# Kernel tuning notes

Measured on AMD Instinct MI355X. Metric: run time of the kernel, lower is better.

## Reference

```python
import jax, jax.numpy as jnp
import numpy as np

EPS = 1e-5

def _layer_norm(x, g, b):
    m = jnp.mean(x, axis=-1, keepdims=True)
    v = jnp.mean((x - m) ** 2, axis=-1, keepdims=True)
    return (x - m) / jnp.sqrt(v + EPS) * g + b

def _dpb(idx, w0, b0, g1, be1, w1, b1, g2, be2, w2, b2, g3, be3, w3, b3):
    # idx: (n, dim, 1) -> (h, n, dim)
    h = idx @ w0 + b0                                   # (n, dim, D)
    h = jax.nn.relu(_layer_norm(h, g1, be1)) @ w1 + b1  # pos1
    h = jax.nn.relu(_layer_norm(h, g2, be2)) @ w2 + b2  # pos2
    h = jax.nn.relu(_layer_norm(h, g3, be3)) @ w3 + b3  # pos3 -> (n, dim, H)
    return jnp.transpose(h, (2, 0, 1))                  # (H, n, dim)

def setup_inputs() -> dict:
    key = jax.random.key(0)
    ks = jax.random.split(key, 6)
    B, H, N, DIM, D = 8, 16, 4096, 64, 64
    s = 0.02
    return {
        "x": jax.random.normal(ks[0], (B, H, N, DIM), jnp.float32),
        "w0": jax.random.normal(ks[1], (1, D), jnp.float32) * s,
        "b0": jnp.zeros((D,), jnp.float32),
        "g1": jnp.ones((D,), jnp.float32),
        "be1": jnp.zeros((D,), jnp.float32),
        "w1": jax.random.normal(ks[2], (D, D), jnp.float32) * s,
        "b1": jnp.zeros((D,), jnp.float32),
        "g2": jnp.ones((D,), jnp.float32),
        "be2": jnp.zeros((D,), jnp.float32),
        "w2": jax.random.normal(ks[3], (D, D), jnp.float32) * s,
        "b2": jnp.zeros((D,), jnp.float32),
        "g3": jnp.ones((D,), jnp.float32),
        "be3": jnp.zeros((D,), jnp.float32),
        "w3": jax.random.normal(ks[4], (D, H), jnp.float32) * s,
        "b3": jnp.zeros((H,), jnp.float32),
    }

def reference(x, w0, b0, g1, be1, w1, b1, g2, be2, w2, b2, g3, be3, w3, b3):
    # DynamicToepliztMultiheadV3 forward (par_type=1, no pad/exp/decay, non-causal)
    n = x.shape[-2]
    dim = x.shape[-1]
    m = n - 1
    dpb_args = (w0, b0, g1, be1, w1, b1, g2, be2, w2, b2, g3, be3, w3, b3)
    scale = 1.0 / (m * dim)
    flat = jnp.arange(1, 1 + m * dim, dtype=x.dtype)
    pos_idx = (flat * scale).reshape(m, dim, 1)
    neg_idx = (-jnp.flip(flat) * scale).reshape(m, dim, 1)  # flip on flat, then reshape (matches torch)
    zero_idx = jnp.zeros((1, dim, 1), x.dtype)
    zero = _dpb(zero_idx, *dpb_args)   # (H, 1, dim)
    pos = _dpb(pos_idx, *dpb_args)     # (H, n-1, dim)
    neg = _dpb(neg_idx, *dpb_args)     # (H, n-1, dim)
    a = jnp.concatenate([zero, pos, zero, neg], axis=1)  # (H, 2n, dim)
    # FFT-based circular (Toeplitz) convolution along seq axis
    y = jnp.fft.rfft(x, 2 * n, axis=-2, norm='ortho')          # (B,H,n+1,dim) complex
    v = jnp.fft.rfft(a, axis=-2)[None]                          # backward norm, as in torch
    out = jnp.fft.irfft(v * y, 2 * n, axis=-2, norm='ortho')[:, :, :n, :]
    return out
```

## Files before the change

### kernel.cpp

```cpp
#include <hip/hip_runtime.h>
#include <math.h>

static const size_t OFF_TW = 0;
static const size_t OFF_V  = 32768;
static const size_t OFF_AT = OFF_V  + (size_t)16 * 64 * 4104 * 8;
static const size_t OFF_ZX = OFF_AT + (size_t)16 * 32 * 8192 * 8;
static const size_t WS_NEED = OFF_ZX + (size_t)128 * 32 * 4096 * 8;

__global__ void __launch_bounds__(256) k_init_tw(float2* __restrict__ tw)
{
    int k = blockIdx.x * 256 + threadIdx.x;
    if (k < 4096) {
        double a = (double)k * (3.14159265358979323846 / 4096.0);
        tw[k] = make_float2((float)cos(a), (float)(-sin(a)));
    }
}

__device__ __forceinline__ void ln_relu_arr(float* b,
                                            const float* __restrict__ g,
                                            const float* __restrict__ be)
{
    float s0 = 0, s1 = 0, s2 = 0, s3 = 0;
    #pragma unroll
    for (int k = 0; k < 64; k += 4) {
        s0 += b[k]; s1 += b[k + 1]; s2 += b[k + 2]; s3 += b[k + 3];
    }
    float m = (s0 + s1 + s2 + s3) * (1.0f / 64.0f);
    float v0 = 0, v1 = 0, v2 = 0, v3 = 0;
    #pragma unroll
    for (int k = 0; k < 64; k += 4) {
        float c0 = b[k] - m, c1 = b[k + 1] - m, c2 = b[k + 2] - m, c3 = b[k + 3] - m;
        v0 = fmaf(c0, c0, v0); v1 = fmaf(c1, c1, v1);
        v2 = fmaf(c2, c2, v2); v3 = fmaf(c3, c3, v3);
    }
    float inv = rsqrtf((v0 + v1 + v2 + v3) * (1.0f / 64.0f) + 1e-5f);
    #pragma unroll
    for (int k = 0; k < 64; ++k)
        b[k] = fmaxf(fmaf((b[k] - m) * inv, g[k], be[k]), 0.0f);
}

__device__ __forceinline__ void matmul64(const float* b, float* o,
                                         const float* __restrict__ w,
                                         const float* __restrict__ bias)
{
    #pragma unroll
    for (int j = 0; j < 64; ++j) o[j] = bias[j];
    #pragma unroll
    for (int k = 0; k < 64; ++k) {
        float bk = b[k];
        const float* wr = w + (k << 6);
        #pragma unroll
        for (int j = 0; j < 64; ++j) o[j] = fmaf(bk, wr[j], o[j]);
    }
}

__global__ void __launch_bounds__(256) k_dpb(
    const float* __restrict__ w0,  const float* __restrict__ b0,
    const float* __restrict__ g1,  const float* __restrict__ be1,
    const float* __restrict__ w1,  const float* __restrict__ b1,
    const float* __restrict__ g2,  const float* __restrict__ be2,
    const float* __restrict__ w2,  const float* __restrict__ b2,
    const float* __restrict__ g3,  const float* __restrict__ be3,
    const float* __restrict__ w3,  const float* __restrict__ b3,
    float* __restrict__ aTf)
{
    int e  = blockIdx.x * 256 + threadIdx.x;
    int r  = e & 8191;
    int dd = e >> 13;
    const float scale = (float)(1.0 / 262080.0);
    float u;
    if (r == 0 || r == 4096) u = 0.0f;
    else if (r < 4096)       u = (float)((r - 1) * 64 + dd + 1) * scale;
    else                     u = -(float)(262080 - ((r - 4097) * 64 + dd)) * scale;

    float b[64], o[64];
    #pragma unroll
    for (int j = 0; j < 64; ++j) b[j] = fmaf(u, w0[j], b0[j]);

    ln_relu_arr(b, g1, be1);
    matmul64(b, o, w1, b1);
    ln_relu_arr(o, g2, be2);
    matmul64(o, b, w2, b2);
    ln_relu_arr(b, g3, be3);

    float f[16];
    #pragma unroll
    for (int j = 0; j < 16; ++j) f[j] = b3[j];
    #pragma unroll
    for (int k = 0; k < 64; ++k) {
        float bk = b[k];
        const float* wr = w3 + (k << 4);
        #pragma unroll
        for (int j = 0; j < 16; ++j) f[j] = fmaf(bk, wr[j], f[j]);
    }
    #pragma unroll
    for (int h = 0; h < 16; ++h) {
        size_t idx = ((size_t)((h << 5) + (dd >> 1)) * 8192 + r) * 2 + (dd & 1);
        aTf[idx] = f[h];
    }
}

__device__ __forceinline__ int sw(int a)
{
    return a ^ ((a >> 4) & 15) ^ ((a >> 8) & 1);
}

__device__ __forceinline__ float2 cmul(float2 a, float2 b)
{
    return make_float2(fmaf(a.x, b.x, -(a.y * b.y)), fmaf(a.x, b.y, a.y * b.x));
}

template<bool INV>
__device__ __forceinline__ float2 twm(float2 a, float wr, float wi)
{
    float i = INV ? -wi : wi;
    return make_float2(fmaf(a.x, wr, -(a.y * i)), fmaf(a.x, i, a.y * wr));
}

template<bool INV>
__device__ __forceinline__ void fft16(float2* z)
{
    const float SQ = 0.70710678118654752440f;
    const float C1 = 0.92387953251128675613f;
    const float S1 = 0.38268343236508977173f;
    #pragma unroll
    for (int b = 0; b < 16; b += 2) {
        float2 u = z[b], t = z[b + 1];
        z[b]     = make_float2(u.x + t.x, u.y + t.y);
        z[b + 1] = make_float2(u.x - t.x, u.y - t.y);
    }
    const float w4r[2] = {1.0f, 0.0f};
    const float w4i[2] = {0.0f, -1.0f};
    #pragma unroll
    for (int b = 0; b < 16; b += 4) {
        #pragma unroll
        for (int j = 0; j < 2; ++j) {
            float2 u = z[b + j];
            float2 t = twm<INV>(z[b + j + 2], w4r[j], w4i[j]);
            z[b + j]     = make_float2(u.x + t.x, u.y + t.y);
            z[b + j + 2] = make_float2(u.x - t.x, u.y - t.y);
        }
    }
    const float w8r[4] = {1.0f, SQ, 0.0f, -SQ};
    const float w8i[4] = {0.0f, -SQ, -1.0f, -SQ};
    #pragma unroll
    for (int b = 0; b < 16; b += 8) {
        #pragma unroll
        for (int j = 0; j < 4; ++j) {
            float2 u = z[b + j];
            float2 t = twm<INV>(z[b + j + 4], w8r[j], w8i[j]);
            z[b + j]     = make_float2(u.x + t.x, u.y + t.y);
            z[b + j + 4] = make_float2(u.x - t.x, u.y - t.y);
        }
    }
    const float wgr[8] = {1.0f, C1, SQ, S1, 0.0f, -S1, -SQ, -C1};
    const float wgi[8] = {0.0f, -S1, -SQ, -C1, -1.0f, -C1, -SQ, -S1};
    #pragma unroll
    for (int j = 0; j < 8; ++j) {
        float2 u = z[j];
        float2 t = twm<INV>(z[j + 8], wgr[j], wgi[j]);
        z[j]     = make_float2(u.x + t.x, u.y + t.y);
        z[j + 8] = make_float2(u.x - t.x, u.y - t.y);
    }
}

template<bool INV>
__device__ __forceinline__ void r16(float2* __restrict__ Z, int base, int j, int L, int s,
                                    const float2* __restrict__ tw)
{
    int addr[16];
    #pragma unroll
    for (int m = 0; m < 16; ++m) addr[m] = sw(base + j + L * m);
    float2 t1 = tw[j * s], t2 = tw[2 * j * s], t4 = tw[4 * j * s], t8 = tw[8 * j * s];
    if (INV) { t1.y = -t1.y; t2.y = -t2.y; t4.y = -t4.y; t8.y = -t8.y; }
    float2 T[16];
    T[1] = t1; T[2] = t2; T[4] = t4; T[8] = t8;
    T[3]  = cmul(t1, t2);   T[5]  = cmul(t1, t4);   T[6]  = cmul(t2, t4);
    T[7]  = cmul(T[3], t4); T[9]  = cmul(t1, t8);   T[10] = cmul(t2, t8);
    T[11] = cmul(T[3], t8); T[12] = cmul(t4, t8);   T[13] = cmul(T[5], t8);
    T[14] = cmul(T[6], t8); T[15] = cmul(T[7], t8);
    const int rv[16] = {0, 8, 4, 12, 2, 10, 6, 14, 1, 9, 5, 13, 3, 11, 7, 15};
    float2 z[16];
    z[0] = Z[addr[0]];
    #pragma unroll
    for (int m = 1; m < 16; ++m) z[m] = cmul(Z[addr[m]], T[rv[m]]);
    fft16<INV>(z);
    #pragma unroll
    for (int q = 0; q < 16; ++q) Z[addr[q]] = z[q];
}

template<int L, bool INV>
__device__ __forceinline__ void reg_stage16(float* xr, float* xi,
                                            const float2* __restrict__ tw)
{
    #pragma unroll
    for (int b = 0; b < 16; b += 2 * L) {
        #pragma unroll
        for (int j = 0; j < L; ++j) {
            float2 w = tw[j * (4096 / L)];
            float wr = w.x, wi = INV ? -w.y : w.y;
            int i0 = b + j, i1 = b + j + L;
            float tr = xr[i1] * wr - xi[i1] * wi;
            float ti = xr[i1] * wi + xi[i1] * wr;
            xr[i1] = xr[i0] - tr; xi[i1] = xi[i0] - ti;
            xr[i0] += tr;         xi[i0] += ti;
        }
    }
}

template<bool INV>
__device__ __forceinline__ void fft8192_lds(float2* __restrict__ Z,
                                            const float2* __restrict__ tw)
{
    const int t  = threadIdx.x;
    const int r9 = (int)(__brev((unsigned)t) >> 23);
    float xr[16], xi[16];
    #pragma unroll
    for (int i = 0; i < 16; ++i) {
        int r4 = (int)(__brev((unsigned)i) >> 28);
        float2 v = Z[sw((r4 << 9) | r9)];
        xr[i] = v.x; xi[i] = v.y;
    }
    __syncthreads();
    reg_stage16<1, INV>(xr, xi, tw);
    reg_stage16<2, INV>(xr, xi, tw);
    reg_stage16<4, INV>(xr, xi, tw);
    reg_stage16<8, INV>(xr, xi, tw);
    #pragma unroll
    for (int i = 0; i < 16; ++i) Z[sw(16 * t + i)] = make_float2(xr[i], xi[i]);
    __syncthreads();
    r16<INV>(Z, (t >> 4) * 256, t & 15, 16, 32, tw);
    __syncthreads();
    r16<INV>(Z, (t >> 8) * 4096, t & 255, 256, 2, tw);
    __syncthreads();
    #pragma unroll
    for (int m = 0; m < 8; ++m) {
        int k = t + 512 * m;
        float2 w = tw[k];
        float wi = INV ? -w.y : w.y;
        int aL = sw(k), aH = sw(k + 4096);
        float2 u = Z[aL], v = Z[aH];
        float tr = fmaf(v.x, w.x, -(v.y * wi));
        float ti = fmaf(v.x, wi, v.y * w.x);
        Z[aL] = make_float2(u.x + tr, u.y + ti);
        Z[aH] = make_float2(u.x - tr, u.y - ti);
    }
    __syncthreads();
}

__global__ void __launch_bounds__(512, 4) k_vfft(const float2* __restrict__ aT,
                                                 const float2* __restrict__ tw,
                                                 float2* __restrict__ V)
{
    __shared__ float2 Z[8192];
    int blk = blockIdx.x;
    int h = blk >> 5, p = blk & 31;
    const float2* ac = aT + (size_t)(h * 32 + p) * 8192;
    int t = threadIdx.x;
    #pragma unroll
    for (int i = 0; i < 16; ++i) {
        int idx = i * 512 + t;
        Z[sw(idx)] = ac[idx];
    }
    __syncthreads();
    fft8192_lds<false>(Z, tw);
    const float s = 1.0f / 8192.0f;
    float2* V0 = V + (size_t)(h * 64 + 2 * p) * 4104;
    float2* V1 = V0 + 4104;
    for (int k = t; k <= 4096; k += 512) {
        int km = (8192 - k) & 8191;
        float2 z1 = Z[sw(k)], z2 = Z[sw(km)];
        float zr1 = z1.x, zi1 = z1.y;
        float zr2 = z2.x, zi2 = -z2.y;
        float a0r = 0.5f * (zr1 + zr2), a0i = 0.5f * (zi1 + zi2);
        float a1r = 0.5f * (zi1 - zi2), a1i = -0.5f * (zr1 - zr2);
        V0[k] = make_float2(a0r * s, a0i * s);
        V1[k] = make_float2(a1r * s, a1i * s);
    }
}

__global__ void __launch_bounds__(256) k_pack_x(const float* __restrict__ x,
                                                float2* __restrict__ zx)
{
    int blk = blockIdx.x;
    int bh = blk >> 7, rt = blk & 127, r0 = rt << 5;
    __shared__ float tile[64][33];
    const float* xp = x + (size_t)bh * 4096 * 64;
    int tid = threadIdx.x;
    #pragma unroll
    for (int i = 0; i < 8; ++i) {
        int idx = i * 256 + tid;
        int rr = idx >> 6, d = idx & 63;
        tile[d][rr] = xp[(size_t)(r0 + rr) * 64 + d];
    }
    __syncthreads();
    float2* zp = zx + (size_t)bh * 32 * 4096;
    #pragma unroll
    for (int i = 0; i < 4; ++i) {
        int idx = i * 256 + tid;
        int p = idx >> 5, rr = idx & 31;
        zp[(size_t)p * 4096 + r0 + rr] = make_float2(tile[2 * p][rr], tile[2 * p + 1][rr]);
    }
}

__global__ void __launch_bounds__(512, 4) k_conv(float2* __restrict__ zx,
                                                 const float2* __restrict__ V,
                                                 const float2* __restrict__ tw)
{
    __shared__ float2 Z[8192];
    int blk = blockIdx.x;
    int bh = blk >> 5, p = blk & 31, h = bh & 15;
    float2* zc = zx + (size_t)blk * 4096;
    int t = threadIdx.x;
    #pragma unroll
    for (int i = 0; i < 8; ++i) {
        int idx = i * 512 + t;
        Z[sw(idx)] = zc[idx];
        Z[sw(idx + 4096)] = make_float2(0.0f, 0.0f);
    }
    __syncthreads();
    fft8192_lds<false>(Z, tw);
    const float2* V0 = V + (size_t)(h * 64 + 2 * p) * 4104;
    const float2* V1 = V0 + 4104;
    for (int k = t; k <= 4096; k += 512) {
        int km = (8192 - k) & 8191;
        float2 z1 = Z[sw(k)], z2 = Z[sw(km)];
        float zr1 = z1.x, zi1 = z1.y;
        float zr2 = z2.x, zi2 = -z2.y;
        float x0r = 0.5f * (zr1 + zr2), x0i = 0.5f * (zi1 + zi2);
        float x1r = 0.5f * (zi1 - zi2), x1i = -0.5f * (zr1 - zr2);
        float2 v0 = V0[k], v1 = V1[k];
        float y0r = v0.x * x0r - v0.y * x0i, y0i = v0.x * x0i + v0.y * x0r;
        float y1r = v1.x * x1r - v1.y * x1i, y1i = v1.x * x1i + v1.y * x1r;
        Z[sw(k)] = make_float2(y0r - y1i, y0i + y1r);
        if (k > 0 && k < 4096)
            Z[sw(km)] = make_float2(y0r + y1i, y1r - y0i);
    }
    __syncthreads();
    fft8192_lds<true>(Z, tw);
    #pragma unroll
    for (int i = 0; i < 8; ++i) {
        int idx = i * 512 + t;
        zc[idx] = Z[sw(idx)];
    }
}

__global__ void __launch_bounds__(256) k_unpack_out(const float2* __restrict__ zo,
                                                    float* __restrict__ out)
{
    int blk = blockIdx.x;
    int bh = blk >> 7, rt = blk & 127, r0 = rt << 5;
    __shared__ float tile[64][33];
    const float2* zp = zo + (size_t)bh * 32 * 4096;
    int tid = threadIdx.x;
    #pragma unroll
    for (int i = 0; i < 4; ++i) {
        int idx = i * 256 + tid;
        int p = idx >> 5, rr = idx & 31;
        float2 v = zp[(size_t)p * 4096 + r0 + rr];
        tile[2 * p][rr] = v.x; tile[2 * p + 1][rr] = v.y;
    }
    __syncthreads();
    float* op = out + (size_t)bh * 4096 * 64;
    #pragma unroll
    for (int i = 0; i < 8; ++i) {
        int idx = i * 256 + tid;
        int rr = idx >> 6, d = idx & 63;
        op[(size_t)(r0 + rr) * 64 + d] = tile[d][rr];
    }
}

extern "C" void kernel_launch(void* const* d_in, const int* in_sizes, int n_in,
                              void* d_out, int out_size, void* d_ws, size_t ws_size,
                              hipStream_t stream)
{
    (void)in_sizes; (void)n_in; (void)out_size;
    const float* x   = (const float*)d_in[0];
    const float* w0  = (const float*)d_in[1];
    const float* b0  = (const float*)d_in[2];
    const float* g1  = (const float*)d_in[3];
    const float* be1 = (const float*)d_in[4];
    const float* w1  = (const float*)d_in[5];
    const float* b1  = (const float*)d_in[6];
    const float* g2  = (const float*)d_in[7];
    const float* be2 = (const float*)d_in[8];
    const float* w2  = (const float*)d_in[9];
    const float* b2  = (const float*)d_in[10];
    const float* g3  = (const float*)d_in[11];
    const float* be3 = (const float*)d_in[12];
    const float* w3  = (const float*)d_in[13];
    const float* b3  = (const float*)d_in[14];
    float* out = (float*)d_out;
    char* ws = (char*)d_ws;
    if (ws_size < WS_NEED) return;

    float2* tw = (float2*)(ws + OFF_TW);
    float2* V  = (float2*)(ws + OFF_V);
    float2* aT = (float2*)(ws + OFF_AT);
    float2* zx = (float2*)(ws + OFF_ZX);

    k_init_tw<<<16, 256, 0, stream>>>(tw);
    k_dpb<<<2048, 256, 0, stream>>>(w0, b0, g1, be1, w1, b1, g2, be2,
                                    w2, b2, g3, be3, w3, b3, (float*)aT);
    k_vfft<<<512, 512, 0, stream>>>(aT, tw, V);
    k_pack_x<<<16384, 256, 0, stream>>>(x, zx);
    k_conv<<<4096, 512, 0, stream>>>(zx, V, tw);
    k_unpack_out<<<16384, 256, 0, stream>>>((const float2*)zx, out);
}
```

Measured before the change: 786.6 us.

## Restructure 8192-point FFT tail as three radix-8 stages instead of radix-16/radix-2

Changes the shared-memory FFT decomposition after the register radix-16 stage from radix-16, radix-16, radix-2 to three radix-8 passes, each thread doing two radix-8 butterflies per pass. The number of passes and barriers stays the same, but each butterfly holds fewer live registers and the separate radix-2 pass over shared memory is folded into the last radix-8 pass. In exchange, each thread now issues two butterflies per pass with twiddle products recomputed for each, and the stage strides change, so shared-memory bank behaviour may differ.

```diff
diff --git a/kernel.cpp b/kernel.cpp
--- a/kernel.cpp
+++ b/kernel.cpp
@@ -118,13 +118,11 @@
 }
 
 template<bool INV>
-__device__ __forceinline__ void fft16(float2* z)
+__device__ __forceinline__ void fft8(float2* z)
 {
     const float SQ = 0.70710678118654752440f;
-    const float C1 = 0.92387953251128675613f;
-    const float S1 = 0.38268343236508977173f;
-    #pragma unroll
-    for (int b = 0; b < 16; b += 2) {
+    #pragma unroll
+    for (int b = 0; b < 8; b += 2) {
         float2 u = z[b], t = z[b + 1];
         z[b]     = make_float2(u.x + t.x, u.y + t.y);
         z[b + 1] = make_float2(u.x - t.x, u.y - t.y);
@@ -132,7 +130,7 @@
     const float w4r[2] = {1.0f, 0.0f};
     const float w4i[2] = {0.0f, -1.0f};
     #pragma unroll
-    for (int b = 0; b < 16; b += 4) {
+    for (int b = 0; b < 8; b += 4) {
         #pragma unroll
         for (int j = 0; j < 2; ++j) {
             float2 u = z[b + j];
@@ -144,49 +142,36 @@
     const float w8r[4] = {1.0f, SQ, 0.0f, -SQ};
     const float w8i[4] = {0.0f, -SQ, -1.0f, -SQ};
     #pragma unroll
-    for (int b = 0; b < 16; b += 8) {
-        #pragma unroll
-        for (int j = 0; j < 4; ++j) {
-            float2 u = z[b + j];
-            float2 t = twm<INV>(z[b + j + 4], w8r[j], w8i[j]);
-            z[b + j]     = make_float2(u.x + t.x, u.y + t.y);
-            z[b + j + 4] = make_float2(u.x - t.x, u.y - t.y);
-        }
-    }
-    const float wgr[8] = {1.0f, C1, SQ, S1, 0.0f, -S1, -SQ, -C1};
-    const float wgi[8] = {0.0f, -S1, -SQ, -C1, -1.0f, -C1, -SQ, -S1};
-    #pragma unroll
-    for (int j = 0; j < 8; ++j) {
+    for (int j = 0; j < 4; ++j) {
         float2 u = z[j];
-        float2 t = twm<INV>(z[j + 8], wgr[j], wgi[j]);
+        float2 t = twm<INV>(z[j + 4], w8r[j], w8i[j]);
         z[j]     = make_float2(u.x + t.x, u.y + t.y);
-        z[j + 8] = make_float2(u.x - t.x, u.y - t.y);
+        z[j + 4] = make_float2(u.x - t.x, u.y - t.y);
     }
 }
 
 template<bool INV>
-__device__ __forceinline__ void r16(float2* __restrict__ Z, int base, int j, int L, int s,
-                                    const float2* __restrict__ tw)
-{
-    int addr[16];
-    #pragma unroll
-    for (int m = 0; m < 16; ++m) addr[m] = sw(base + j + L * m);
-    float2 t1 = tw[j * s], t2 = tw[2 * j * s], t4 = tw[4 * j * s], t8 = tw[8 * j * s];
-    if (INV) { t1.y = -t1.y; t2.y = -t2.y; t4.y = -t4.y; t8.y = -t8.y; }
-    float2 T[16];
-    T[1] = t1; T[2] = t2; T[4] = t4; T[8] = t8;
-    T[3]  = cmul(t1, t2);   T[5]  = cmul(t1, t4);   T[6]  = cmul(t2, t4);
-    T[7]  = cmul(T[3], t4); T[9]  = cmul(t1, t8);   T[10] = cmul(t2, t8);
-    T[11] = cmul(T[3], t8); T[12] = cmul(t4, t8);   T[13] = cmul(T[5], t8);
-    T[14] = cmul(T[6], t8); T[15] = cmul(T[7], t8);
-    const int rv[16] = {0, 8, 4, 12, 2, 10, 6, 14, 1, 9, 5, 13, 3, 11, 7, 15};
-    float2 z[16];
+__device__ __forceinline__ void r8(float2* __restrict__ Z, int base, int j, int L, int s,
+                                   const float2* __restrict__ tw)
+{
+    int addr[8];
+    #pragma unroll
+    for (int m = 0; m < 8; ++m) addr[m] = sw(base + j + L * m);
+    float2 t1 = tw[j * s], t2 = tw[2 * j * s], t4 = tw[4 * j * s];
+    if (INV) { t1.y = -t1.y; t2.y = -t2.y; t4.y = -t4.y; }
+    float2 T3 = cmul(t1, t2), T5 = cmul(t1, t4), T6 = cmul(t2, t4), T7 = cmul(T3, t4);
+    float2 z[8];
     z[0] = Z[addr[0]];
-    #pragma unroll
-    for (int m = 1; m < 16; ++m) z[m] = cmul(Z[addr[m]], T[rv[m]]);
-    fft16<INV>(z);
-    #pragma unroll
-    for (int q = 0; q < 16; ++q) Z[addr[q]] = z[q];
+    z[1] = cmul(Z[addr[1]], t4);
+    z[2] = cmul(Z[addr[2]], t2);
+    z[3] = cmul(Z[addr[3]], T6);
+    z[4] = cmul(Z[addr[4]], t1);
+    z[5] = cmul(Z[addr[5]], T5);
+    z[6] = cmul(Z[addr[6]], T3);
+    z[7] = cmul(Z[addr[7]], T7);
+    fft8<INV>(z);
+    #pragma unroll
+    for (int q = 0; q < 8; ++q) Z[addr[q]] = z[q];
 }
 
 template<int L, bool INV>
@@ -229,22 +214,14 @@
     #pragma unroll
     for (int i = 0; i < 16; ++i) Z[sw(16 * t + i)] = make_float2(xr[i], xi[i]);
     __syncthreads();
-    r16<INV>(Z, (t >> 4) * 256, t & 15, 16, 32, tw);
-    __syncthreads();
-    r16<INV>(Z, (t >> 8) * 4096, t & 255, 256, 2, tw);
-    __syncthreads();
-    #pragma unroll
-    for (int m = 0; m < 8; ++m) {
-        int k = t + 512 * m;
-        float2 w = tw[k];
-        float wi = INV ? -w.y : w.y;
-        int aL = sw(k), aH = sw(k + 4096);
-        float2 u = Z[aL], v = Z[aH];
-        float tr = fmaf(v.x, w.x, -(v.y * wi));
-        float ti = fmaf(v.x, wi, v.y * w.x);
-        Z[aL] = make_float2(u.x + tr, u.y + ti);
-        Z[aH] = make_float2(u.x - tr, u.y - ti);
-    }
+    r8<INV>(Z, (t >> 4) * 128, t & 15, 16, 64, tw);
+    r8<INV>(Z, ((t + 512) >> 4) * 128, t & 15, 16, 64, tw);
+    __syncthreads();
+    r8<INV>(Z, (t >> 7) * 1024, t & 127, 128, 8, tw);
+    r8<INV>(Z, ((t + 512) >> 7) * 1024, (t + 512) & 127, 128, 8, tw);
+    __syncthreads();
+    r8<INV>(Z, 0, t, 1024, 1, tw);
+    r8<INV>(Z, 0, t + 512, 1024, 1, tw);
     __syncthreads();
 }
 
```

After: 779.5 us. Within noise of the previous version (-0.9%).
